# Kernel optimization log

Measured on AMD Instinct MI355X. Metric: run time of the kernel, lower is better.

Reference implementation:

```python
import jax, jax.numpy as jnp
import numpy as np

DIM = 192
HEADS = 6
HEAD_DIM = DIM // HEADS  # 32
N = 64                   # prod(window_size) = 4*4*4
BW = 4096                # num_windows * B
NEG = -1e9               # finite stand-in for -inf additive mask


def setup_inputs() -> dict:
    key = jax.random.key(0)
    k_x, k_m, k_qkv, k_p, k_pb = jax.random.split(key, 5)
    x = jax.random.normal(k_x, (BW, N, N and 192))  # (BW, N, C)
    x = jax.random.normal(k_x, (BW, N, DIM), dtype=jnp.float32)
    # Shifted-window style additive mask: block-diagonal groups of tokens.
    # Each window gets a random group id per token; tokens attend only within
    # their group (0), cross-group gets NEG. Diagonal always allowed.
    gid = jax.random.randint(k_m, (BW, N), 0, 3)  # (BW, N) group ids in {0,1,2}
    same = gid[:, :, None] == gid[:, None, :]     # (BW, N, N) bool
    mask = jnp.where(same, 0.0, NEG).astype(jnp.float32)[:, None, :, :]  # (BW,1,N,N)
    w_qkv = jax.random.normal(k_qkv, (3 * DIM, DIM), dtype=jnp.float32) * (DIM ** -0.5)
    w_proj = jax.random.normal(k_p, (DIM, DIM), dtype=jnp.float32) * (DIM ** -0.5)
    b_proj = jax.random.normal(k_pb, (DIM,), dtype=jnp.float32) * 0.02
    return {"x": x, "mask": mask, "w_qkv": w_qkv, "w_proj": w_proj, "b_proj": b_proj}


def reference(x, mask, w_qkv, w_proj, b_proj):
    b, n, c = x.shape
    scale = HEAD_DIM ** -0.5
    # qkv linear (no bias) then split: 'b n (three heads c) -> three b heads n c'
    qkv = jnp.einsum('bnc,dc->bnd', x, w_qkv)               # (b, n, 3*C)
    qkv = qkv.reshape(b, n, 3, HEADS, HEAD_DIM)
    qkv = jnp.transpose(qkv, (2, 0, 3, 1, 4))               # (3, b, heads, n, hd)
    q, k, v = qkv[0], qkv[1], qkv[2]
    q = q * scale
    # scaled_dot_product_attention with additive mask (scale=1 since q pre-scaled)
    scores = jnp.einsum('bhqd,bhkd->bhqk', q, k) + mask     # (b, heads, n, n)
    probs = jax.nn.softmax(scores, axis=-1)
    out = jnp.einsum('bhqk,bhkd->bhqd', probs, v)           # (b, heads, n, hd)
    # 'b k n c -> b n (k c)'
    out = jnp.transpose(out, (0, 2, 1, 3)).reshape(b, n, c)
    # output projection (bias=True in nn.Linear default)
    return jnp.einsum('bnc,dc->bnd', out, w_proj) + b_proj
```

## Files before the change

### kernel.cpp

```cpp
#include <hip/hip_runtime.h>

#define NTOK 64
#define DIM 192
#define HD 32

#define RS  200
#define VTS 68
#define WQN (576 * DIM)
#define WPN (DIM * DIM)

typedef __attribute__((ext_vector_type(8))) short short8;
typedef __attribute__((ext_vector_type(4))) float floatx4;
typedef __attribute__((ext_vector_type(2))) unsigned int uint2v;

__device__ __forceinline__ short f2bf(float f) {
    union { float f; unsigned int u; } c; c.f = f;
    unsigned int r = (c.u + 0x7FFFu + ((c.u >> 16) & 1u)) >> 16;
    return (short)(unsigned short)r;
}

__device__ __forceinline__ unsigned pkbf(float a, float b) {
    unsigned ua = __float_as_uint(a); ua += 0x7FFFu + ((ua >> 16) & 1u);
    unsigned ub = __float_as_uint(b); ub += 0x7FFFu + ((ub >> 16) & 1u);
    return __builtin_amdgcn_perm(ub, ua, 0x07060302u);
}

__device__ __forceinline__ short8 cvt8(const float* p) {
    const float4* v = reinterpret_cast<const float4*>(p);
    float4 lo = v[0], hi = v[1];
    union { unsigned u[4]; short8 s; } r;
    r.u[0] = pkbf(lo.x, lo.y);
    r.u[1] = pkbf(lo.z, lo.w);
    r.u[2] = pkbf(hi.x, hi.y);
    r.u[3] = pkbf(hi.z, hi.w);
    return r.s;
}

__device__ __forceinline__ short8 qshuf(floatx4 v0, floatx4 v1, int lane) {
    const int q = lane >> 4;
    const unsigned p0a = pkbf(v0[0], v0[1]);
    const unsigned p0b = pkbf(v0[2], v0[3]);
    const unsigned p1a = pkbf(v1[0], v1[1]);
    const unsigned p1b = pkbf(v1[2], v1[3]);
    const int s0 = (lane & 15) | ((q & 1) << 5);
    const int s1 = s0 + 16;
    const unsigned l0 = (unsigned)__shfl((int)p0a, s0);
    const unsigned h0 = (unsigned)__shfl((int)p1a, s0);
    const unsigned l1 = (unsigned)__shfl((int)p0b, s0);
    const unsigned h1 = (unsigned)__shfl((int)p1b, s0);
    const unsigned l2 = (unsigned)__shfl((int)p0a, s1);
    const unsigned h2 = (unsigned)__shfl((int)p1a, s1);
    const unsigned l3 = (unsigned)__shfl((int)p0b, s1);
    const unsigned h3 = (unsigned)__shfl((int)p1b, s1);
    const bool hi = q >= 2;
    union { unsigned u[4]; short8 s; } ret;
    ret.u[0] = hi ? h0 : l0;
    ret.u[1] = hi ? h1 : l1;
    ret.u[2] = hi ? h2 : l2;
    ret.u[3] = hi ? h3 : l3;
    return ret.s;
}

__global__ void wprep(const float* __restrict__ wqkv, const float* __restrict__ wproj,
                      short* __restrict__ wqb, short* __restrict__ wpb) {
    const int i = blockIdx.x * 256 + (int)threadIdx.x;
    for (int e = i; e < WQN; e += 192 * 256) {
        float v = wqkv[e];
        if (e < DIM * DIM) v *= 0.17677669529663688f;
        wqb[e] = f2bf(v);
    }
    for (int e = i; e < WPN; e += 192 * 256) wpb[e] = f2bf(wproj[e]);
}

template <int WS>
__global__ __launch_bounds__(256, 3)
void wattn_fused(const float* __restrict__ x, const float* __restrict__ mask,
                 const float* __restrict__ wqkv, const float* __restrict__ wproj,
                 const float* __restrict__ bproj, float* __restrict__ out,
                 const short* __restrict__ wqb, const short* __restrict__ wpb) {
    __shared__ short ksm[NTOK * RS];
    __shared__ short vsT[DIM * VTS];

    const int bw   = blockIdx.x;
    const int tid  = (int)threadIdx.x;
    const int wave = tid >> 6;
    const int lane = tid & 63;
    const int r    = lane & 15;
    const int q    = lane >> 4;

    const float* xb = x + (size_t)bw * (NTOK * DIM);

    auto ldq = [&](int off) -> short8 {
        if constexpr (WS) return *reinterpret_cast<const short8*>(wqb + off);
        else              return cvt8(wqkv + off);
    };
    auto ldp = [&](int off) -> short8 {
        if constexpr (WS) return *reinterpret_cast<const short8*>(wpb + off);
        else              return cvt8(wproj + off);
    };

    {
        short8 a[4][6];
        #pragma unroll
        for (int mt = 0; mt < 4; ++mt) {
            #pragma unroll
            for (int s = 0; s < 6; ++s)
                a[mt][s] = cvt8(xb + (mt * 16 + r) * DIM + s * 32 + q * 8);
        }

        if (wave < 2) {
            const int cb = wave * 96;
            #pragma unroll
            for (int nt = 0; nt < 6; ++nt) {
                const int dk = cb + nt * 16;
                floatx4 acc[4];
                #pragma unroll
                for (int mt = 0; mt < 4; ++mt) acc[mt] = (floatx4){0.f, 0.f, 0.f, 0.f};
                #pragma unroll
                for (int s = 0; s < 6; ++s) {
                    const short8 b8 = ldq((DIM + dk + r) * DIM + s * 32 + q * 8);
                    #pragma unroll
                    for (int mt = 0; mt < 4; ++mt)
                        acc[mt] = __builtin_amdgcn_mfma_f32_16x16x32_bf16(b8, a[mt][s], acc[mt], 0, 0, 0);
                }
                #pragma unroll
                for (int mt = 0; mt < 4; ++mt) {
                    uint2v u;
                    u.x = pkbf(acc[mt][0], acc[mt][1]);
                    u.y = pkbf(acc[mt][2], acc[mt][3]);
                    *reinterpret_cast<uint2v*>(ksm + (mt * 16 + r) * RS + dk + q * 4) = u;
                }
            }
        } else {
            const int cb = (wave - 2) * 96;
            #pragma unroll
            for (int nt = 0; nt < 6; ++nt) {
                const int dv = cb + nt * 16;
                floatx4 acc[4];
                #pragma unroll
                for (int mt = 0; mt < 4; ++mt) acc[mt] = (floatx4){0.f, 0.f, 0.f, 0.f};
                #pragma unroll
                for (int s = 0; s < 6; ++s) {
                    const short8 b8 = ldq((2 * DIM + dv + r) * DIM + s * 32 + q * 8);
                    #pragma unroll
                    for (int mt = 0; mt < 4; ++mt)
                        acc[mt] = __builtin_amdgcn_mfma_f32_16x16x32_bf16(a[mt][s], b8, acc[mt], 0, 0, 0);
                }
                #pragma unroll
                for (int mt = 0; mt < 4; ++mt) {
                    uint2v u;
                    u.x = pkbf(acc[mt][0], acc[mt][1]);
                    u.y = pkbf(acc[mt][2], acc[mt][3]);
                    *reinterpret_cast<uint2v*>(vsT + (dv + r) * VTS + mt * 16 + q * 4) = u;
                }
            }
        }
    }
    __builtin_amdgcn_sched_barrier(0);

    short8 bq[3][2];
    #pragma unroll
    for (int i = 0; i < 3; ++i) {
        const int uu = wave * 3 + i, h = uu >> 1, half = uu & 1;
        floatx4 qa[2][2];
        #pragma unroll
        for (int dt = 0; dt < 2; ++dt) {
            #pragma unroll
            for (int qt = 0; qt < 2; ++qt) qa[dt][qt] = (floatx4){0.f, 0.f, 0.f, 0.f};
        }
        #pragma unroll
        for (int s = 0; s < 6; ++s) {
            const short8 w0 = ldq((h * HD + r) * DIM + s * 32 + q * 8);
            const short8 w1 = ldq((h * HD + 16 + r) * DIM + s * 32 + q * 8);
            #pragma unroll
            for (int qt = 0; qt < 2; ++qt) {
                const short8 xf = cvt8(xb + ((half * 2 + qt) * 16 + r) * DIM + s * 32 + q * 8);
                qa[0][qt] = __builtin_amdgcn_mfma_f32_16x16x32_bf16(w0, xf, qa[0][qt], 0, 0, 0);
                qa[1][qt] = __builtin_amdgcn_mfma_f32_16x16x32_bf16(w1, xf, qa[1][qt], 0, 0, 0);
            }
        }
        if constexpr (!WS) {
            #pragma unroll
            for (int dt = 0; dt < 2; ++dt)
                #pragma unroll
                for (int qt = 0; qt < 2; ++qt)
                    #pragma unroll
                    for (int g = 0; g < 4; ++g)
                        qa[dt][qt][g] *= 0.17677669529663688f;
        }
        bq[i][0] = qshuf(qa[0][0], qa[1][0], lane);
        bq[i][1] = qshuf(qa[0][1], qa[1][1], lane);
    }
    __syncthreads();

    const float* mb  = mask + (size_t)bw * (NTOK * NTOK);
    const float* mbl = mb + 256 * q + r;
    uint2v obf[3][2][2];

    #pragma unroll
    for (int i = 0; i < 3; ++i) {
        const int uu = wave * 3 + i, h = uu >> 1, half = uu & 1;

        float mv[2][4][4];
        #pragma unroll
        for (int qt = 0; qt < 2; ++qt)
            #pragma unroll
            for (int kt = 0; kt < 4; ++kt)
                #pragma unroll
                for (int g = 0; g < 4; ++g)
                    mv[qt][kt][g] = mbl[kt * 1024 + g * 64 + half * 32 + qt * 16];

        short8 bk[4];
        #pragma unroll
        for (int kt = 0; kt < 4; ++kt)
            bk[kt] = *reinterpret_cast<const short8*>(ksm + (kt * 16 + r) * RS + h * HD + q * 8);

        floatx4 sa[4][2];
        #pragma unroll
        for (int kt = 0; kt < 4; ++kt) {
            #pragma unroll
            for (int qt = 0; qt < 2; ++qt) {
                floatx4 z = (floatx4){0.f, 0.f, 0.f, 0.f};
                sa[kt][qt] = __builtin_amdgcn_mfma_f32_16x16x32_bf16(bk[kt], bq[i][qt], z, 0, 0, 0);
            }
        }
        #pragma unroll
        for (int kt = 0; kt < 4; ++kt)
            #pragma unroll
            for (int qt = 0; qt < 2; ++qt)
                #pragma unroll
                for (int g = 0; g < 4; ++g)
                    sa[kt][qt][g] += mv[qt][kt][g];

        float rinv[2];
        #pragma unroll
        for (int qt = 0; qt < 2; ++qt) {
            float mx = sa[0][qt][0];
            #pragma unroll
            for (int kt = 0; kt < 4; ++kt)
                #pragma unroll
                for (int g = 0; g < 4; ++g) mx = fmaxf(mx, sa[kt][qt][g]);
            mx = fmaxf(mx, __shfl_xor(mx, 16));
            mx = fmaxf(mx, __shfl_xor(mx, 32));
            float sm = 0.f;
            #pragma unroll
            for (int kt = 0; kt < 4; ++kt) {
                #pragma unroll
                for (int g = 0; g < 4; ++g) {
                    float p = __expf(sa[kt][qt][g] - mx);
                    sa[kt][qt][g] = p;
                    sm += p;
                }
            }
            sm += __shfl_xor(sm, 16);
            sm += __shfl_xor(sm, 32);
            rinv[qt] = 1.0f / sm;
        }

        short8 ap[2][2];
        #pragma unroll
        for (int qt = 0; qt < 2; ++qt) {
            #pragma unroll
            for (int kk = 0; kk < 2; ++kk)
                ap[qt][kk] = qshuf(sa[2 * kk][qt], sa[2 * kk + 1][qt], lane);
        }

        short8 bv[2][2];
        #pragma unroll
        for (int nv = 0; nv < 2; ++nv)
            #pragma unroll
            for (int kk = 0; kk < 2; ++kk)
                bv[nv][kk] = *reinterpret_cast<const short8*>(
                    vsT + (h * HD + nv * 16 + r) * VTS + kk * 32 + q * 8);

        #pragma unroll
        for (int qt = 0; qt < 2; ++qt) {
            #pragma unroll
            for (int nv = 0; nv < 2; ++nv) {
                floatx4 o = (floatx4){0.f, 0.f, 0.f, 0.f};
                o = __builtin_amdgcn_mfma_f32_16x16x32_bf16(bv[nv][0], ap[qt][0], o, 0, 0, 0);
                o = __builtin_amdgcn_mfma_f32_16x16x32_bf16(bv[nv][1], ap[qt][1], o, 0, 0, 0);
                uint2v u;
                u.x = pkbf(o[0] * rinv[qt], o[1] * rinv[qt]);
                u.y = pkbf(o[2] * rinv[qt], o[3] * rinv[qt]);
                obf[i][qt][nv] = u;
            }
        }
    }

    __syncthreads();
    #pragma unroll
    for (int i = 0; i < 3; ++i) {
        const int uu = wave * 3 + i, h = uu >> 1, half = uu & 1;
        #pragma unroll
        for (int qt = 0; qt < 2; ++qt)
            #pragma unroll
            for (int nv = 0; nv < 2; ++nv)
                *reinterpret_cast<uint2v*>(
                    ksm + (half * 32 + qt * 16 + r) * RS + h * HD + nv * 16 + q * 4) = obf[i][qt][nv];
    }
    __syncthreads();

    short8 ao[4][6];
    #pragma unroll
    for (int mt = 0; mt < 4; ++mt) {
        #pragma unroll
        for (int s = 0; s < 6; ++s)
            ao[mt][s] = *reinterpret_cast<const short8*>(ksm + (mt * 16 + r) * RS + s * 32 + q * 8);
    }

    float* ob = out + (size_t)bw * (NTOK * DIM);
    const int D0 = wave * 48;
    #pragma unroll
    for (int nt = 0; nt < 3; ++nt) {
        const int d0 = D0 + nt * 16;
        const float4 b4 = *reinterpret_cast<const float4*>(bproj + d0 + q * 4);
        floatx4 acc[4];
        #pragma unroll
        for (int mt = 0; mt < 4; ++mt) acc[mt] = (floatx4){b4.x, b4.y, b4.z, b4.w};
        #pragma unroll
        for (int s = 0; s < 6; ++s) {
            const short8 w8 = ldp((d0 + r) * DIM + s * 32 + q * 8);
            #pragma unroll
            for (int mt = 0; mt < 4; ++mt)
                acc[mt] = __builtin_amdgcn_mfma_f32_16x16x32_bf16(w8, ao[mt][s], acc[mt], 0, 0, 0);
        }
        #pragma unroll
        for (int mt = 0; mt < 4; ++mt) {
            float4 st;
            st.x = acc[mt][0]; st.y = acc[mt][1]; st.z = acc[mt][2]; st.w = acc[mt][3];
            *reinterpret_cast<float4*>(ob + (mt * 16 + r) * DIM + d0 + q * 4) = st;
        }
    }
}

extern "C" void kernel_launch(void* const* d_in, const int* in_sizes, int n_in,
                              void* d_out, int out_size, void* d_ws, size_t ws_size,
                              hipStream_t stream) {
    const float* x    = (const float*)d_in[0];
    const float* mask = (const float*)d_in[1];
    const float* wqkv = (const float*)d_in[2];
    const float* wp   = (const float*)d_in[3];
    const float* bp   = (const float*)d_in[4];
    float* out = (float*)d_out;
    const int nblocks = in_sizes[0] / (NTOK * DIM);
    const size_t need = (size_t)(WQN + WPN) * sizeof(short);
    if (d_ws != nullptr && ws_size >= need) {
        short* wqb = (short*)d_ws;
        short* wpb = wqb + WQN;
        wprep<<<192, 256, 0, stream>>>(wqkv, wp, wqb, wpb);
        wattn_fused<1><<<nblocks, 256, 0, stream>>>(x, mask, wqkv, wp, bp, out, wqb, wpb);
    } else {
        wattn_fused<0><<<nblocks, 256, 0, stream>>>(x, mask, wqkv, wp, bp, out, nullptr, nullptr);
    }
}
```

Baseline: 687.3 us.

## Merge Q projection into attention loop, add separate output LDS buffer

Folds the per-unit Q projection into the attention loop, so the Q fragments and output fragments no longer have to stay live in registers across all three units. Attention output is written straight to a new dedicated LDS buffer, which removes one barrier and the register-held obf array. Several loops are set to unroll 1 to cut register pressure, and the launch bound drops from 3 to 2 blocks per CU. The risk is that the extra LDS and the lower occupancy bound leave less latency hiding, and the rolled loops may lose instruction-level overlap.

```diff
diff --git a/kernel.cpp b/kernel.cpp
--- a/kernel.cpp
+++ b/kernel.cpp
@@ -73,13 +73,14 @@
 }
 
 template <int WS>
-__global__ __launch_bounds__(256, 3)
+__global__ __launch_bounds__(256, 2)
 void wattn_fused(const float* __restrict__ x, const float* __restrict__ mask,
                  const float* __restrict__ wqkv, const float* __restrict__ wproj,
                  const float* __restrict__ bproj, float* __restrict__ out,
                  const short* __restrict__ wqb, const short* __restrict__ wpb) {
     __shared__ short ksm[NTOK * RS];
     __shared__ short vsT[DIM * VTS];
+    __shared__ short osm[NTOK * RS];
 
     const int bw   = blockIdx.x;
     const int tid  = (int)threadIdx.x;
@@ -109,10 +110,9 @@
         }
 
         if (wave < 2) {
-            const int cb = wave * 96;
-            #pragma unroll
+            #pragma unroll 1
             for (int nt = 0; nt < 6; ++nt) {
-                const int dk = cb + nt * 16;
+                const int dk = wave * 96 + nt * 16;
                 floatx4 acc[4];
                 #pragma unroll
                 for (int mt = 0; mt < 4; ++mt) acc[mt] = (floatx4){0.f, 0.f, 0.f, 0.f};
@@ -132,10 +132,9 @@
                 }
             }
         } else {
-            const int cb = (wave - 2) * 96;
-            #pragma unroll
+            #pragma unroll 1
             for (int nt = 0; nt < 6; ++nt) {
-                const int dv = cb + nt * 16;
+                const int dv = (wave - 2) * 96 + nt * 16;
                 floatx4 acc[4];
                 #pragma unroll
                 for (int mt = 0; mt < 4; ++mt) acc[mt] = (floatx4){0.f, 0.f, 0.f, 0.f};
@@ -157,17 +156,29 @@
         }
     }
     __builtin_amdgcn_sched_barrier(0);
-
-    short8 bq[3][2];
-    #pragma unroll
+    __syncthreads();
+
+    const float* mb  = mask + (size_t)bw * (NTOK * NTOK);
+    const float* mbl = mb + 256 * q + r;
+
+    #pragma unroll 1
     for (int i = 0; i < 3; ++i) {
         const int uu = wave * 3 + i, h = uu >> 1, half = uu & 1;
+
+        float mv[2][4][4];
+        #pragma unroll
+        for (int qt = 0; qt < 2; ++qt)
+            #pragma unroll
+            for (int kt = 0; kt < 4; ++kt)
+                #pragma unroll
+                for (int g = 0; g < 4; ++g)
+                    mv[qt][kt][g] = mbl[kt * 1024 + g * 64 + half * 32 + qt * 16];
+
         floatx4 qa[2][2];
         #pragma unroll
-        for (int dt = 0; dt < 2; ++dt) {
+        for (int dt = 0; dt < 2; ++dt)
             #pragma unroll
             for (int qt = 0; qt < 2; ++qt) qa[dt][qt] = (floatx4){0.f, 0.f, 0.f, 0.f};
-        }
         #pragma unroll
         for (int s = 0; s < 6; ++s) {
             const short8 w0 = ldq((h * HD + r) * DIM + s * 32 + q * 8);
@@ -188,27 +199,8 @@
                     for (int g = 0; g < 4; ++g)
                         qa[dt][qt][g] *= 0.17677669529663688f;
         }
-        bq[i][0] = qshuf(qa[0][0], qa[1][0], lane);
-        bq[i][1] = qshuf(qa[0][1], qa[1][1], lane);
-    }
-    __syncthreads();
-
-    const float* mb  = mask + (size_t)bw * (NTOK * NTOK);
-    const float* mbl = mb + 256 * q + r;
-    uint2v obf[3][2][2];
-
-    #pragma unroll
-    for (int i = 0; i < 3; ++i) {
-        const int uu = wave * 3 + i, h = uu >> 1, half = uu & 1;
-
-        float mv[2][4][4];
-        #pragma unroll
-        for (int qt = 0; qt < 2; ++qt)
-            #pragma unroll
-            for (int kt = 0; kt < 4; ++kt)
-                #pragma unroll
-                for (int g = 0; g < 4; ++g)
-                    mv[qt][kt][g] = mbl[kt * 1024 + g * 64 + half * 32 + qt * 16];
+        short8 bq0 = qshuf(qa[0][0], qa[1][0], lane);
+        short8 bq1 = qshuf(qa[0][1], qa[1][1], lane);
 
         short8 bk[4];
         #pragma unroll
@@ -218,11 +210,9 @@
         floatx4 sa[4][2];
         #pragma unroll
         for (int kt = 0; kt < 4; ++kt) {
-            #pragma unroll
-            for (int qt = 0; qt < 2; ++qt) {
-                floatx4 z = (floatx4){0.f, 0.f, 0.f, 0.f};
-                sa[kt][qt] = __builtin_amdgcn_mfma_f32_16x16x32_bf16(bk[kt], bq[i][qt], z, 0, 0, 0);
-            }
+            floatx4 z = (floatx4){0.f, 0.f, 0.f, 0.f};
+            sa[kt][0] = __builtin_amdgcn_mfma_f32_16x16x32_bf16(bk[kt], bq0, z, 0, 0, 0);
+            sa[kt][1] = __builtin_amdgcn_mfma_f32_16x16x32_bf16(bk[kt], bq1, z, 0, 0, 0);
         }
         #pragma unroll
         for (int kt = 0; kt < 4; ++kt)
@@ -283,21 +273,10 @@
                 uint2v u;
                 u.x = pkbf(o[0] * rinv[qt], o[1] * rinv[qt]);
                 u.y = pkbf(o[2] * rinv[qt], o[3] * rinv[qt]);
-                obf[i][qt][nv] = u;
-            }
-        }
-    }
-
-    __syncthreads();
-    #pragma unroll
-    for (int i = 0; i < 3; ++i) {
-        const int uu = wave * 3 + i, h = uu >> 1, half = uu & 1;
-        #pragma unroll
-        for (int qt = 0; qt < 2; ++qt)
-            #pragma unroll
-            for (int nv = 0; nv < 2; ++nv)
                 *reinterpret_cast<uint2v*>(
-                    ksm + (half * 32 + qt * 16 + r) * RS + h * HD + nv * 16 + q * 4) = obf[i][qt][nv];
+                    osm + (half * 32 + qt * 16 + r) * RS + h * HD + nv * 16 + q * 4) = u;
+            }
+        }
     }
     __syncthreads();
 
@@ -306,14 +285,13 @@
     for (int mt = 0; mt < 4; ++mt) {
         #pragma unroll
         for (int s = 0; s < 6; ++s)
-            ao[mt][s] = *reinterpret_cast<const short8*>(ksm + (mt * 16 + r) * RS + s * 32 + q * 8);
+            ao[mt][s] = *reinterpret_cast<const short8*>(osm + (mt * 16 + r) * RS + s * 32 + q * 8);
     }
 
     float* ob = out + (size_t)bw * (NTOK * DIM);
-    const int D0 = wave * 48;
-    #pragma unroll
+    #pragma unroll 1
     for (int nt = 0; nt < 3; ++nt) {
-        const int d0 = D0 + nt * 16;
+        const int d0 = wave * 48 + nt * 16;
         const float4 b4 = *reinterpret_cast<const float4*>(bproj + d0 + q * 4);
         floatx4 acc[4];
         #pragma unroll
```

Result: no change. 700.7 us (+2.0%).
